# Kernel optimization log

Measured on AMD Instinct MI355X. Metric: run time of the kernel, lower is better.

## Reference

```python
import jax, jax.numpy as jnp
import numpy as np
from jax import lax

EPS = 1e-5

def setup_inputs() -> dict:
    key = jax.random.key(0)
    k1, k2 = jax.random.split(key)
    x = jax.random.normal(k1, (32, 256, 56, 56), dtype=jnp.float32)
    W = jax.random.normal(k2, (256, 256, 3, 3), dtype=jnp.float32) * 0.05  # real-valued latent weights
    gamma = jnp.ones((256,), dtype=jnp.float32)
    beta = jnp.zeros((256,), dtype=jnp.float32)
    return {"x": x, "W": W, "gamma": gamma, "beta": beta}

def reference(x, W, gamma, beta):
    # Binarize weights to {-1,+1} (deterministic sign, as in BinaryConnect)
    Wb = jnp.sign(W)
    # Conv: stride 1, padding 1, NCHW/OIHW -> [B, 256, 56, 56]
    y = lax.conv_general_dilated(x, Wb, window_strides=(1, 1),
                                 padding=[(1, 1), (1, 1)],
                                 dimension_numbers=("NCHW", "OIHW", "NCHW"))
    # BatchNorm2d (training mode: batch statistics, biased variance)
    mean = jnp.mean(y, axis=(0, 2, 3), keepdims=True)
    var = jnp.mean((y - mean) ** 2, axis=(0, 2, 3), keepdims=True)
    y = (y - mean) * lax.rsqrt(var + EPS)
    y = y * gamma[None, :, None, None] + beta[None, :, None, None]
    # ReLU
    y = jnp.maximum(y, 0.0)
    # MaxPool2d kernel 2, stride 2 -> [B, 256, 28, 28]
    y = lax.reduce_window(y, -jnp.inf, lax.max,
                          window_dimensions=(1, 1, 2, 2),
                          window_strides=(1, 1, 2, 2),
                          padding="VALID")
    return y
```

## Files before the change

kernel.cpp:

```cpp
#include <hip/hip_runtime.h>
#include <stdint.h>

typedef int i32x4  __attribute__((ext_vector_type(4)));
typedef int i32x16 __attribute__((ext_vector_type(16)));
typedef unsigned short u16;

#define M_TOTAL   100352
#define PLANE_I8  1722368L
#define WQ_OFF    27557888L
#define Y_OFF     28147712L
#define STATS_OFF 79527936L
#define QS   21.166666f
#define SYQ  0.047244094f
#define SC16 0.755905509f

__global__ void prep_w(const float* __restrict__ W, char* __restrict__ wq) {
  int idx = blockIdx.x * 256 + threadIdx.x;
  int e  = idx & 15;
  int co = (idx >> 4) & 255;
  int ck = idx >> 12;
  int f  = ck >> 4;
  int ci = ((ck & 15) << 4) | e;
  int kh = (f * 11) >> 5;
  int kw = f - kh * 3;
  float v = W[((co * 256 + ci) * 3 + kh) * 3 + kw];
  wq[idx] = v < 0.0f ? (char)-1 : (char)1;
}

__global__ void border_zero(char* __restrict__ xq) {
  int idx = blockIdx.x * 256 + threadIdx.x;
  int g = idx & 15;
  int p = (idx >> 4) % 228;
  int n = (idx >> 4) / 228;
  int h, w;
  if (p < 58)       { h = 0;  w = p; }
  else if (p < 116) { h = 57; w = p - 58; }
  else { int q = p - 116; h = 1 + (q >> 1); w = 57 * (q & 1); }
  long r = ((long)n * 58 + h) * 58 + w;
  *(uint4*)(xq + g * PLANE_I8 + r * 16) = make_uint4(0, 0, 0, 0);
}

__global__ void prep_x(const float* __restrict__ x, char* __restrict__ xq) {
  int b = blockIdx.x;
  int cblk = b & 3;
  int nh = b >> 2;
  int hp = nh % 28, n = nh / 28;
  __shared__ float tile[64][114];
  int tid = threadIdx.x;
  const float* src = x + (((long)n * 256 + cblk * 64) * 56 + hp * 2) * 56;
#pragma unroll
  for (int i = 0; i < 7; ++i) {
    int idx = i * 256 + tid;
    int cl = idx / 28, rem = idx - cl * 28;
    int h2 = rem / 14, v4 = rem - h2 * 14;
    float4 d = *(const float4*)(src + (long)cl * 3136 + h2 * 56 + v4 * 4);
    float* tp = &tile[cl][h2 * 57 + v4 * 4];
    tp[0] = d.x; tp[1] = d.y; tp[2] = d.z; tp[3] = d.w;
  }
  __syncthreads();
  char* base = xq + (long)(cblk * 4) * PLANE_I8
               + (((long)n * 58 + hp * 2 + 1) * 58 + 1) * 16;
#pragma unroll
  for (int i = 0; i < 2; ++i) {
    int idx = i * 256 + tid;
    if (idx < 448) {
      int g4 = idx & 3, h2 = (idx >> 2) & 1, wq_ = idx >> 3;
      union { uint4 u; char c[16]; } d;
#pragma unroll
      for (int e = 0; e < 16; ++e) {
        int q = __float2int_rn(tile[g4 * 16 + e][h2 * 57 + wq_] * QS);
        q = q > 127 ? 127 : (q < -127 ? -127 : q);
        d.c[e] = (char)q;
      }
      *(uint4*)(base + (long)g4 * PLANE_I8 + (h2 * 58 + wq_) * 16) = d.u;
    }
  }
}

__global__ __launch_bounds__(256, 2) void conv_gemm(
    const char* __restrict__ xq, const char* __restrict__ wq,
    short* __restrict__ y16, float* __restrict__ stats) {
  const int tid = threadIdx.x;
  const int w = tid >> 6, l = tid & 63;
  const int gm = blockIdx.x;
  const int l31 = l & 31, lh = l >> 5;

  long voffA0, voffA1, voffA2, voffA3;
  {
    long vs[4];
#pragma unroll
    for (int rb = 0; rb < 4; ++rb) {
      int gr = gm * 128 + rb * 32 + l31;
      int n = gr / 3136, rem = gr - n * 3136;
      int hh = rem / 56, wx = rem - hh * 56;
      vs[rb] = (long)lh * PLANE_I8 + (((long)n * 58 + hh) * 58 + wx) * 16;
    }
    voffA0 = vs[0]; voffA1 = vs[1]; voffA2 = vs[2]; voffA3 = vs[3];
  }
  const long voffB = (long)lh * 4096 + ((w << 6) + l31) * 16;

  i32x4 aC[2][4], aN[2][4], bC[2][2], bN[2][2];
  i32x16 acc[4][2] = {};

#define LOADA(F, CS, DST)                                                    \
  {                                                                          \
    const int kh_ = ((F) * 11) >> 5;                                         \
    const int kw_ = (F) - kh_ * 3;                                           \
    const char* ba = xq + (long)(CS) * 4 * PLANE_I8 + (kh_ * 58 + kw_) * 16; \
    DST[0][0] = *(const i32x4*)(ba + voffA0);                                \
    DST[0][1] = *(const i32x4*)(ba + voffA1);                                \
    DST[0][2] = *(const i32x4*)(ba + voffA2);                                \
    DST[0][3] = *(const i32x4*)(ba + voffA3);                                \
    const char* ba1 = ba + 2 * PLANE_I8;                                     \
    DST[1][0] = *(const i32x4*)(ba1 + voffA0);                               \
    DST[1][1] = *(const i32x4*)(ba1 + voffA1);                               \
    DST[1][2] = *(const i32x4*)(ba1 + voffA2);                               \
    DST[1][3] = *(const i32x4*)(ba1 + voffA3);                               \
  }
#define LOADB(F, CS, DST)                                                    \
  {                                                                          \
    const char* bb = wq + (long)(((F) << 4) + ((CS) << 2)) * 4096 + voffB;   \
    DST[0][0] = *(const i32x4*)(bb);                                         \
    DST[0][1] = *(const i32x4*)(bb + 512);                                   \
    DST[1][0] = *(const i32x4*)(bb + 8192);                                  \
    DST[1][1] = *(const i32x4*)(bb + 8192 + 512);                            \
  }
#define MFMA16(A, B)                                                         \
  {                                                                          \
    _Pragma("unroll")                                                        \
    for (int kc = 0; kc < 2; ++kc)                                           \
      _Pragma("unroll")                                                      \
      for (int rb = 0; rb < 4; ++rb) {                                       \
        acc[rb][0] = __builtin_amdgcn_mfma_i32_32x32x32_i8(                  \
            A[kc][rb], B[kc][0], acc[rb][0], 0, 0, 0);                       \
        acc[rb][1] = __builtin_amdgcn_mfma_i32_32x32x32_i8(                  \
            A[kc][rb], B[kc][1], acc[rb][1], 0, 0, 0);                       \
      }                                                                      \
  }

  LOADA(0, 0, aC);
  LOADB(0, 0, bC);

  int fN = 1, csN = 0;
  int fC = 2, csC = 0;
  for (int i = 0; i < 18; ++i) {
    LOADA(fN, csN, aN); LOADB(fN, csN, bN);
    fN += 2; if (fN >= 9) { fN -= 9; ++csN; }
    MFMA16(aC, bC);
    if (i < 17) {
      LOADA(fC, csC, aC); LOADB(fC, csC, bC);
      fC += 2; if (fC >= 9) { fC -= 9; ++csC; }
    }
    MFMA16(aN, bN);
  }
#undef LOADA
#undef LOADB
#undef MFMA16

#pragma unroll
  for (int cb = 0; cb < 2; ++cb) {
    float s = 0.f, q = 0.f;
#pragma unroll
    for (int rb = 0; rb < 4; ++rb)
#pragma unroll
      for (int j = 0; j < 16; ++j) {
        float v = SYQ * (float)acc[rb][cb][j];
        s += v; q += v * v;
      }
    s += __shfl_xor(s, 32, 64);
    q += __shfl_xor(q, 32, 64);
    if (lh == 0) {
      int col = (w << 6) + cb * 32 + l31;
      atomicAdd(&stats[col], s);
      atomicAdd(&stats[256 + col], q);
    }
  }

  const long rbase = (long)gm * 128;
#pragma unroll
  for (int rb = 0; rb < 4; ++rb)
#pragma unroll
    for (int j = 0; j < 16; ++j) {
      long rr = rbase + rb * 32 + (j & 3) + 8 * (j >> 2) + 4 * lh;
      short* dst = y16 + rr * 256 + (w << 6) + l31;
      dst[0]  = (short)((acc[rb][0][j] + 8) >> 4);
      dst[32] = (short)((acc[rb][1][j] + 8) >> 4);
    }
}

__global__ void bn_stats(const float* __restrict__ stats, const float* __restrict__ gamma,
                         const float* __restrict__ beta, float* __restrict__ sc) {
  int c = threadIdx.x;
  const float inv = 1.0f / (float)M_TOTAL;
  float mean = stats[c] * inv;
  float var  = stats[256 + c] * inv - mean * mean;
  float s = gamma[c] * rsqrtf(var + 1e-5f);
  sc[c] = s * SC16;
  sc[256 + c] = beta[c] - mean * s;
}

__global__ void bn_pool(const short* __restrict__ y16, const float* __restrict__ sc,
                        float* __restrict__ out) {
  int b = blockIdx.x;
  int ho = b % 28, n = b / 28;
  __shared__ short t[256][113];
  __shared__ float ssc[256], ssb[256];
  int tid = threadIdx.x;
  ssc[tid] = sc[tid];
  ssb[tid] = sc[256 + tid];
  const short* src = y16 + (((long)n * 56 + ho * 2) * 56) * 256;
#pragma unroll
  for (int i = 0; i < 14; ++i) {
    int v = i * 256 + tid;
    int cv = v & 31, hw = v >> 5;
    union { uint4 u; short h[8]; } d;
    d.u = *(const uint4*)(src + (long)hw * 256 + cv * 8);
#pragma unroll
    for (int e = 0; e < 8; ++e) t[cv * 8 + e][hw] = d.h[e];
  }
  __syncthreads();
  float* dst = out + (long)n * 200704 + ho * 28;
#pragma unroll
  for (int i = 0; i < 7; ++i) {
    int oidx = i * 256 + tid;
    int co = oidx / 7, wq4 = oidx - co * 7;
    float s = ssc[co], bb = ssb[co];
    int w0 = wq4 * 8;
    float4 o;
    {
      float r0 = fmaf(s, (float)t[co][w0 + 0], bb), r1 = fmaf(s, (float)t[co][w0 + 1], bb);
      float r2 = fmaf(s, (float)t[co][56 + w0 + 0], bb), r3 = fmaf(s, (float)t[co][56 + w0 + 1], bb);
      o.x = fmaxf(fmaxf(fmaxf(r0, r1), fmaxf(r2, r3)), 0.f);
    }
    {
      float r0 = fmaf(s, (float)t[co][w0 + 2], bb), r1 = fmaf(s, (float)t[co][w0 + 3], bb);
      float r2 = fmaf(s, (float)t[co][56 + w0 + 2], bb), r3 = fmaf(s, (float)t[co][56 + w0 + 3], bb);
      o.y = fmaxf(fmaxf(fmaxf(r0, r1), fmaxf(r2, r3)), 0.f);
    }
    {
      float r0 = fmaf(s, (float)t[co][w0 + 4], bb), r1 = fmaf(s, (float)t[co][w0 + 5], bb);
      float r2 = fmaf(s, (float)t[co][56 + w0 + 4], bb), r3 = fmaf(s, (float)t[co][56 + w0 + 5], bb);
      o.z = fmaxf(fmaxf(fmaxf(r0, r1), fmaxf(r2, r3)), 0.f);
    }
    {
      float r0 = fmaf(s, (float)t[co][w0 + 6], bb), r1 = fmaf(s, (float)t[co][w0 + 7], bb);
      float r2 = fmaf(s, (float)t[co][56 + w0 + 6], bb), r3 = fmaf(s, (float)t[co][56 + w0 + 7], bb);
      o.w = fmaxf(fmaxf(fmaxf(r0, r1), fmaxf(r2, r3)), 0.f);
    }
    *(float4*)(dst + (long)co * 784 + wq4 * 4) = o;
  }
}

extern "C" void kernel_launch(void* const* d_in, const int* in_sizes, int n_in,
                              void* d_out, int out_size, void* d_ws, size_t ws_size,
                              hipStream_t stream) {
  const float* x     = (const float*)d_in[0];
  const float* W     = (const float*)d_in[1];
  const float* gamma = (const float*)d_in[2];
  const float* beta  = (const float*)d_in[3];
  float* out = (float*)d_out;
  char* ws = (char*)d_ws;
  char*  xq    = ws;
  char*  wq    = ws + WQ_OFF;
  short* y16   = (short*)(ws + Y_OFF);
  float* stats = (float*)(ws + STATS_OFF);

  hipMemsetAsync(stats, 0, 512 * sizeof(float), stream);
  hipLaunchKernelGGL(border_zero, dim3(456), dim3(256), 0, stream, xq);
  hipLaunchKernelGGL(prep_w, dim3(2304), dim3(256), 0, stream, W, wq);
  hipLaunchKernelGGL(prep_x, dim3(32 * 28 * 4), dim3(256), 0, stream, x, xq);
  hipLaunchKernelGGL(conv_gemm, dim3(784), dim3(256), 0, stream, xq, wq, y16, stats);
  hipLaunchKernelGGL(bn_stats, dim3(1), dim3(256), 0, stream, stats, gamma, beta, stats + 512);
  hipLaunchKernelGGL(bn_pool, dim3(32 * 28), dim3(256), 0, stream, y16, stats + 512, out);
}
```

Baseline: 138.1 us.

## Split conv GEMM tiles into 128x128 with 2x2 waves and triple-buffered loads

The conv GEMM block tile changes from 128 rows x 256 columns with each wave owning 64 columns to 128x128, with a 2x2 wave grid where each wave computes 64x64. The grid doubles to 1568 blocks. The register pipeline goes from double to triple buffering of A/B fragments, issuing loads three filter taps ahead. Fewer accumulators per wave should free registers and add memory-level parallelism, at the cost of loading the activation tile twice across the column halves and a lower MFMA-to-load ratio per wave.

```diff
diff --git a/kernel.cpp b/kernel.cpp
--- a/kernel.cpp
+++ b/kernel.cpp
@@ -3,7 +3,6 @@
 
 typedef int i32x4  __attribute__((ext_vector_type(4)));
 typedef int i32x16 __attribute__((ext_vector_type(16)));
-typedef unsigned short u16;
 
 #define M_TOTAL   100352
 #define PLANE_I8  1722368L
@@ -82,25 +81,28 @@
     short* __restrict__ y16, float* __restrict__ stats) {
   const int tid = threadIdx.x;
   const int w = tid >> 6, l = tid & 63;
-  const int gm = blockIdx.x;
+  const int gm = blockIdx.x >> 1;
+  const int gn = blockIdx.x & 1;
+  const int wm = w >> 1, wn = w & 1;
   const int l31 = l & 31, lh = l >> 5;
 
-  long voffA0, voffA1, voffA2, voffA3;
+  long voffA0, voffA1;
   {
-    long vs[4];
-#pragma unroll
-    for (int rb = 0; rb < 4; ++rb) {
-      int gr = gm * 128 + rb * 32 + l31;
+    long vs[2];
+#pragma unroll
+    for (int rb = 0; rb < 2; ++rb) {
+      int gr = gm * 128 + wm * 64 + rb * 32 + l31;
       int n = gr / 3136, rem = gr - n * 3136;
       int hh = rem / 56, wx = rem - hh * 56;
       vs[rb] = (long)lh * PLANE_I8 + (((long)n * 58 + hh) * 58 + wx) * 16;
     }
-    voffA0 = vs[0]; voffA1 = vs[1]; voffA2 = vs[2]; voffA3 = vs[3];
-  }
-  const long voffB = (long)lh * 4096 + ((w << 6) + l31) * 16;
-
-  i32x4 aC[2][4], aN[2][4], bC[2][2], bN[2][2];
-  i32x16 acc[4][2] = {};
+    voffA0 = vs[0]; voffA1 = vs[1];
+  }
+  const long voffB = (long)lh * 4096 + (gn * 128 + wn * 64 + l31) * 16;
+
+  i32x4 a0[2][2], a1[2][2], a2[2][2];
+  i32x4 b0[2][2], b1[2][2], b2[2][2];
+  i32x16 acc[2][2] = {};
 
 #define LOADA(F, CS, DST)                                                    \
   {                                                                          \
@@ -109,13 +111,9 @@
     const char* ba = xq + (long)(CS) * 4 * PLANE_I8 + (kh_ * 58 + kw_) * 16; \
     DST[0][0] = *(const i32x4*)(ba + voffA0);                                \
     DST[0][1] = *(const i32x4*)(ba + voffA1);                                \
-    DST[0][2] = *(const i32x4*)(ba + voffA2);                                \
-    DST[0][3] = *(const i32x4*)(ba + voffA3);                                \
     const char* ba1 = ba + 2 * PLANE_I8;                                     \
     DST[1][0] = *(const i32x4*)(ba1 + voffA0);                               \
     DST[1][1] = *(const i32x4*)(ba1 + voffA1);                               \
-    DST[1][2] = *(const i32x4*)(ba1 + voffA2);                               \
-    DST[1][3] = *(const i32x4*)(ba1 + voffA3);                               \
   }
 #define LOADB(F, CS, DST)                                                    \
   {                                                                          \
@@ -125,12 +123,12 @@
     DST[1][0] = *(const i32x4*)(bb + 8192);                                  \
     DST[1][1] = *(const i32x4*)(bb + 8192 + 512);                            \
   }
-#define MFMA16(A, B)                                                         \
+#define MFMA8(A, B)                                                          \
   {                                                                          \
     _Pragma("unroll")                                                        \
     for (int kc = 0; kc < 2; ++kc)                                           \
       _Pragma("unroll")                                                      \
-      for (int rb = 0; rb < 4; ++rb) {                                       \
+      for (int rb = 0; rb < 2; ++rb) {                                       \
         acc[rb][0] = __builtin_amdgcn_mfma_i32_32x32x32_i8(                  \
             A[kc][rb], B[kc][0], acc[rb][0], 0, 0, 0);                       \
         acc[rb][1] = __builtin_amdgcn_mfma_i32_32x32x32_i8(                  \
@@ -138,30 +136,37 @@
       }                                                                      \
   }
 
-  LOADA(0, 0, aC);
-  LOADB(0, 0, bC);
-
-  int fN = 1, csN = 0;
-  int fC = 2, csC = 0;
-  for (int i = 0; i < 18; ++i) {
-    LOADA(fN, csN, aN); LOADB(fN, csN, bN);
-    fN += 2; if (fN >= 9) { fN -= 9; ++csN; }
-    MFMA16(aC, bC);
-    if (i < 17) {
-      LOADA(fC, csC, aC); LOADB(fC, csC, bC);
-      fC += 2; if (fC >= 9) { fC -= 9; ++csC; }
-    }
-    MFMA16(aN, bN);
+  LOADA(0, 0, a0); LOADB(0, 0, b0);
+  LOADA(1, 0, a1); LOADB(1, 0, b1);
+  LOADA(2, 0, a2); LOADB(2, 0, b2);
+  int f0 = 3, cs0 = 0, f1 = 4, cs1 = 0, f2 = 5, cs2 = 0;
+
+  for (int i = 0; i < 12; ++i) {
+    MFMA8(a0, b0);
+    if (i < 11) {
+      LOADA(f0, cs0, a0); LOADB(f0, cs0, b0);
+      f0 += 3; if (f0 >= 9) { f0 -= 9; ++cs0; }
+    }
+    MFMA8(a1, b1);
+    if (i < 11) {
+      LOADA(f1, cs1, a1); LOADB(f1, cs1, b1);
+      f1 += 3; if (f1 >= 9) { f1 -= 9; ++cs1; }
+    }
+    MFMA8(a2, b2);
+    if (i < 11) {
+      LOADA(f2, cs2, a2); LOADB(f2, cs2, b2);
+      f2 += 3; if (f2 >= 9) { f2 -= 9; ++cs2; }
+    }
   }
 #undef LOADA
 #undef LOADB
-#undef MFMA16
+#undef MFMA8
 
 #pragma unroll
   for (int cb = 0; cb < 2; ++cb) {
     float s = 0.f, q = 0.f;
 #pragma unroll
-    for (int rb = 0; rb < 4; ++rb)
+    for (int rb = 0; rb < 2; ++rb)
 #pragma unroll
       for (int j = 0; j < 16; ++j) {
         float v = SYQ * (float)acc[rb][cb][j];
@@ -170,19 +175,20 @@
     s += __shfl_xor(s, 32, 64);
     q += __shfl_xor(q, 32, 64);
     if (lh == 0) {
-      int col = (w << 6) + cb * 32 + l31;
+      int col = gn * 128 + wn * 64 + cb * 32 + l31;
       atomicAdd(&stats[col], s);
       atomicAdd(&stats[256 + col], q);
     }
   }
 
-  const long rbase = (long)gm * 128;
-#pragma unroll
-  for (int rb = 0; rb < 4; ++rb)
+  const long rbase = (long)gm * 128 + wm * 64;
+  const int  cbase = gn * 128 + wn * 64 + l31;
+#pragma unroll
+  for (int rb = 0; rb < 2; ++rb)
 #pragma unroll
     for (int j = 0; j < 16; ++j) {
       long rr = rbase + rb * 32 + (j & 3) + 8 * (j >> 2) + 4 * lh;
-      short* dst = y16 + rr * 256 + (w << 6) + l31;
+      short* dst = y16 + rr * 256 + cbase;
       dst[0]  = (short)((acc[rb][0][j] + 8) >> 4);
       dst[32] = (short)((acc[rb][1][j] + 8) >> 4);
     }
@@ -269,7 +275,7 @@
   hipLaunchKernelGGL(border_zero, dim3(456), dim3(256), 0, stream, xq);
   hipLaunchKernelGGL(prep_w, dim3(2304), dim3(256), 0, stream, W, wq);
   hipLaunchKernelGGL(prep_x, dim3(32 * 28 * 4), dim3(256), 0, stream, x, xq);
-  hipLaunchKernelGGL(conv_gemm, dim3(784), dim3(256), 0, stream, xq, wq, y16, stats);
+  hipLaunchKernelGGL(conv_gemm, dim3(1568), dim3(256), 0, stream, xq, wq, y16, stats);
   hipLaunchKernelGGL(bn_stats, dim3(1), dim3(256), 0, stream, stats, gamma, beta, stats + 512);
   hipLaunchKernelGGL(bn_pool, dim3(32 * 28), dim3(256), 0, stream, y16, stats + 512, out);
 }
```

Measured after the change: 140.4 us. About the same (+1.6%).
